# Performance work log

Measured on AMD Instinct MI355X. Metric: run time of the kernel, lower is better.

## Reference

```python
import jax, jax.numpy as jnp
import numpy as np

B, N, HID = 8, 1024, 768
HEADS, LORA, HDIM = 12, 256, 64


def setup_inputs() -> dict:
    key = jax.random.key(0)
    k1, k2, k3 = jax.random.split(key, 3)
    hidden_states = jax.random.normal(k1, (B, N, HID), dtype=jnp.float32)
    attention_mask = jnp.ones((B, N), dtype=jnp.int32)
    # torch Linear weights are [out_features, in_features]
    Wt = jax.random.normal(k2, (HEADS, LORA, HID), dtype=jnp.float32) * (HID ** -0.5)
    Wa = jax.random.normal(k3, (HEADS, HDIM, LORA), dtype=jnp.float32) * (LORA ** -0.5)
    return {"hidden_states": hidden_states, "attention_mask": attention_mask,
            "Wt": Wt, "Wa": Wa}


def reference(hidden_states, attention_mask, Wt, Wa):
    # Per-head LoRA projection, batched over heads instead of a Python loop.
    # t: [b, h, n, head_dim]; repeat(1,1,3) in the original makes q = k = v = t.
    scale = hidden_states.shape[-1] ** -0.5  # input_dim ** -0.5
    t = jnp.einsum('bnd,hld->bhnl', hidden_states, Wt)
    t = jnp.einsum('bhnl,hel->bhne', t, Wa)
    scores = jnp.einsum('bhid,bhjd->bhij', t, t) * scale
    scores = jnp.where(attention_mask[:, None, None, :] == 0, -jnp.inf, scores)
    attn = jax.nn.softmax(scores, axis=-1)
    out = jnp.einsum('bhij,bhjd->bhid', attn, t)  # [b, h, n, d]
    b, h, n, d = out.shape
    return out.transpose(0, 2, 1, 3).reshape(b, n, h * d)
```

## Files before the change

### kernel.cpp

```cpp
#include <hip/hip_runtime.h>
#include <math.h>

#define BATCH 8
#define SEQ   1024
#define HID_  768
#define HEADS 12
#define LORA  256
#define HDIM  64

#define SCALE      0.03608439182435161f
#define SCALE_LOG2 0.05205863235888918f

typedef _Float16 f16_t;
typedef _Float16 f16x2 __attribute__((ext_vector_type(2)));
typedef _Float16 f16x4 __attribute__((ext_vector_type(4)));
typedef _Float16 f16x8 __attribute__((ext_vector_type(8)));
typedef float    f32x4 __attribute__((ext_vector_type(4)));

#define GLD16(g, l) __builtin_amdgcn_global_load_lds( \
    (const __attribute__((address_space(1))) void*)(g), \
    (__attribute__((address_space(3))) void*)(l), 16, 0, 0)

#define SW(c, r) ((((c) ^ ((r) & 7)) << 3))

#define N4_HS (BATCH * SEQ * HID_ / 4)

__global__ __launch_bounds__(256) void prep_kernel(
    const float4* __restrict__ hs, const float* __restrict__ Wt,
    const float* __restrict__ Wa, f16x4* __restrict__ hs_f,
    f16_t* __restrict__ w_f)
{
    __shared__ float s_a[64][68];
    __shared__ float s_b[64][36];

    const int tid = threadIdx.x;

    if (blockIdx.x >= 288) {
        int i0 = (blockIdx.x - 288) * 256 + tid;
        int stride = (gridDim.x - 288) * 256;
        for (int i = i0; i < N4_HS; i += stride) {
            float4 v = hs[i];
            f16x4 o = {(f16_t)v.x, (f16_t)v.y, (f16_t)v.z, (f16_t)v.w};
            hs_f[i] = o;
        }
        return;
    }

    const int bid = blockIdx.x;
    const int h   = bid / 24;
    const int d0  = (bid % 24) * 32;
    const int ty  = tid >> 4;
    const int tx  = tid & 15;

    const float* wa_g = Wa + (size_t)h * HDIM * LORA;
    const float* wt_g = Wt + (size_t)h * LORA * HID_;

    float acc[4][2] = {{0.f, 0.f}, {0.f, 0.f}, {0.f, 0.f}, {0.f, 0.f}};

    for (int kc = 0; kc < 4; ++kc) {
        const int l0 = kc * 64;
        if (kc) __syncthreads();
        #pragma unroll
        for (int k = 0; k < 4; ++k) {
            int u = tid + k * 256;
            int r = u >> 4, c4 = (u & 15) * 4;
            *(float4*)&s_a[r][c4] = *(const float4*)&wa_g[(size_t)r * LORA + l0 + c4];
        }
        #pragma unroll
        for (int k = 0; k < 2; ++k) {
            int u = tid + k * 256;
            int r = u >> 3, c4 = (u & 7) * 4;
            *(float4*)&s_b[r][c4] = *(const float4*)&wt_g[(size_t)(l0 + r) * HID_ + d0 + c4];
        }
        __syncthreads();

        #pragma unroll 8
        for (int l = 0; l < 64; ++l) {
            float a0 = s_a[ty * 4 + 0][l];
            float a1 = s_a[ty * 4 + 1][l];
            float a2 = s_a[ty * 4 + 2][l];
            float a3 = s_a[ty * 4 + 3][l];
            float b0 = s_b[l][tx * 2 + 0];
            float b1 = s_b[l][tx * 2 + 1];
            acc[0][0] = fmaf(a0, b0, acc[0][0]); acc[0][1] = fmaf(a0, b1, acc[0][1]);
            acc[1][0] = fmaf(a1, b0, acc[1][0]); acc[1][1] = fmaf(a1, b1, acc[1][1]);
            acc[2][0] = fmaf(a2, b0, acc[2][0]); acc[2][1] = fmaf(a2, b1, acc[2][1]);
            acc[3][0] = fmaf(a3, b0, acc[3][0]); acc[3][1] = fmaf(a3, b1, acc[3][1]);
        }
    }

    f16_t* wg = w_f + (size_t)h * HDIM * HID_;
    #pragma unroll
    for (int i = 0; i < 4; ++i) {
        int e = ty * 4 + i;
        f16x2 o = {(f16_t)acc[i][0], (f16_t)acc[i][1]};
        *(f16x2*)&wg[(size_t)e * HID_ + d0 + tx * 2] = o;
    }
}

__global__ __launch_bounds__(256, 3) void gemm_t(
    const f16_t* __restrict__ hs_f, const f16_t* __restrict__ w_f,
    f16_t* __restrict__ t_f, f16_t* __restrict__ tT_f)
{
    __shared__ __attribute__((aligned(16))) char smem[49152];
    f16_t* s_hs = (f16_t*)smem;
    f16_t* s_wt = (f16_t*)(smem + 32768);
    f16_t* s_ob = (f16_t*)smem;

    const int bid   = blockIdx.x;
    const int ntile = bid & 7;
    const int h     = (bid >> 3) % HEADS;
    const int b     = bid / (8 * HEADS);
    const int n0    = ntile * 128;
    const int tid   = threadIdx.x;
    const int w     = tid >> 6;
    const int lane  = tid & 63;
    const int q     = lane >> 4;
    const int mr    = lane & 15;
    const int lrow  = lane >> 3;
    const int gswz  = (((lane & 7) ^ lrow) & 7) * 8;

    const f16_t* hs_g = hs_f + ((size_t)b * SEQ + n0) * HID_;
    const f16_t* w_g  = w_f + (size_t)h * HDIM * HID_;

    const f32x4 z4 = {0.f, 0.f, 0.f, 0.f};
    f32x4 acc[2][4];
    #pragma unroll
    for (int mt = 0; mt < 2; ++mt)
        #pragma unroll
        for (int et = 0; et < 4; ++et) acc[mt][et] = z4;

    auto STAGE = [&](int buf, int rd) {
        const int k0 = rd * 64;
        f16_t* sa = s_hs + buf * (128 * 64);
        f16_t* sb = s_wt + buf * (64 * 64);
        #pragma unroll
        for (int tt = 0; tt < 4; ++tt) {
            int r0 = w * 32 + tt * 8;
            GLD16(hs_g + (size_t)(r0 + lrow) * HID_ + k0 + gswz, sa + r0 * 64);
        }
        #pragma unroll
        for (int tt = 0; tt < 2; ++tt) {
            int r0 = w * 16 + tt * 8;
            GLD16(w_g + (size_t)(r0 + lrow) * HID_ + k0 + gswz, sb + r0 * 64);
        }
    };

    auto COMPUTE = [&](int buf) {
        const f16_t* sa = s_hs + buf * (128 * 64);
        const f16_t* sb = s_wt + buf * (64 * 64);
        #pragma unroll
        for (int ks = 0; ks < 2; ++ks) {
            f16x8 a_[2], b_[4];
            #pragma unroll
            for (int mt = 0; mt < 2; ++mt)
                a_[mt] = *(const f16x8*)(sa + (w * 32 + mt * 16 + mr) * 64 + SW(ks * 4 + q, mr));
            #pragma unroll
            for (int et = 0; et < 4; ++et)
                b_[et] = *(const f16x8*)(sb + (et * 16 + mr) * 64 + SW(ks * 4 + q, mr));
            #pragma unroll
            for (int mt = 0; mt < 2; ++mt)
                #pragma unroll
                for (int et = 0; et < 4; ++et)
                    acc[mt][et] = __builtin_amdgcn_mfma_f32_16x16x32_f16(a_[mt], b_[et], acc[mt][et], 0, 0, 0);
        }
    };

    STAGE(0, 0);
    __syncthreads();
    #pragma unroll 1
    for (int rr = 0; rr < 6; ++rr) {
        STAGE(1, 2 * rr + 1);
        COMPUTE(0);
        __syncthreads();
        if (rr < 5) STAGE(0, 2 * rr + 2);
        COMPUTE(1);
        __syncthreads();
    }

    #pragma unroll
    for (int mt = 0; mt < 2; ++mt) {
        #pragma unroll
        for (int et = 0; et < 4; ++et) {
            #pragma unroll
            for (int r = 0; r < 4; ++r) {
                int row = w * 32 + mt * 16 + q * 4 + r;
                int col = et * 16 + mr;
                s_ob[row * 72 + col] = (f16_t)acc[mt][et][r];
            }
        }
    }
    __syncthreads();

    f16_t* tg = t_f + (((size_t)b * HEADS + h) * SEQ + n0) * HDIM;
    #pragma unroll
    for (int k = 0; k < 4; ++k) {
        int u = tid + k * 256;
        int row = u >> 3, c8 = (u & 7) * 8;
        *(f16x8*)&tg[row * 64 + c8] = *(const f16x8*)&s_ob[row * 72 + c8];
    }
    f16_t* tTg = tT_f + ((size_t)b * HEADS + h) * SEQ * HDIM;
    #pragma unroll
    for (int k = 0; k < 4; ++k) {
        int u = tid + k * 256;
        int e = u & 63, n8 = (u >> 6) * 8;
        f16x8 v;
        #pragma unroll
        for (int j = 0; j < 8; ++j) v[j] = s_ob[(n8 + j) * 72 + e];
        *(f16x8*)&tTg[(size_t)e * SEQ + n0 + n8] = v;
    }
}

__global__ __launch_bounds__(256, 3) void attn_mfma(
    const f16_t* __restrict__ t_f, const f16_t* __restrict__ tT_f,
    const int* __restrict__ mask, float* __restrict__ out)
{
    __shared__ __attribute__((aligned(16))) char smem[34816];
    f16_t* s_k = (f16_t*)smem;
    f16_t* s_v = (f16_t*)(smem + 8192);
    f16_t* s_p = (f16_t*)(smem + 16384);
    float* s_m = (float*)smem;

    const int bid  = blockIdx.x;
    const int bh   = bid % (BATCH * HEADS);
    const int it   = bid / (BATCH * HEADS);
    const int h    = bh % HEADS;
    const int b    = bh / HEADS;
    const int i0   = it * 128;
    const int tid  = threadIdx.x;
    const int w    = tid >> 6;
    const int lane = tid & 63;
    const int q    = lane >> 4;
    const int mr   = lane & 15;
    const int lrow = lane >> 3;
    const int gswz = (((lane & 7) ^ lrow) & 7) * 8;
    const int ih   = w >> 1;
    const int jh   = w & 1;

    const size_t bh_off = ((size_t)b * HEADS + h) * SEQ * HDIM;
    const f16_t* th = t_f + bh_off;
    const f16_t* vh = tT_f + bh_off;
    const int* mk = mask + (size_t)b * SEQ;

    f16x8 qf[4][2];
    #pragma unroll
    for (int mt = 0; mt < 4; ++mt)
        #pragma unroll
        for (int ks = 0; ks < 2; ++ks) {
            f16x8 v = *(const f16x8*)(th + (size_t)(i0 + ih * 64 + mt * 16 + mr) * 64
                                      + ks * 32 + q * 8);
            #pragma unroll
            for (int j = 0; j < 8; ++j) v[j] = v[j] * (f16_t)SCALE_LOG2;
            qf[mt][ks] = v;
        }

    const f32x4 z4 = {0.f, 0.f, 0.f, 0.f};
    float l_[4] = {0.f, 0.f, 0.f, 0.f};
    f32x4 oT[4][4];
    #pragma unroll
    for (int mt = 0; mt < 4; ++mt)
        #pragma unroll
        for (int et = 0; et < 4; ++et) oT[mt][et] = z4;

    for (int jt6 = 0; jt6 < 16; ++jt6) {
        const int j0 = jt6 * 64;
        __syncthreads();
        #pragma unroll
        for (int t2 = 0; t2 < 2; ++t2) {
            int r0 = w * 16 + t2 * 8;
            GLD16(th + (size_t)(j0 + r0 + lrow) * 64 + gswz,  s_k + r0 * 64);
            GLD16(vh + (size_t)(r0 + lrow) * SEQ + j0 + gswz, s_v + r0 * 64);
        }
        __syncthreads();

        #pragma unroll
        for (int jt = 0; jt < 2; ++jt) {
            int4 mv = *(const int4*)(mk + j0 + jh * 32 + jt * 16 + q * 4);
            f32x4 bias = {(mv.x == 0) ? -60000.f : 0.f,
                          (mv.y == 0) ? -60000.f : 0.f,
                          (mv.z == 0) ? -60000.f : 0.f,
                          (mv.w == 0) ? -60000.f : 0.f};
            f32x4 st[4] = {bias, bias, bias, bias};
            __builtin_amdgcn_s_setprio(1);
            #pragma unroll
            for (int ks = 0; ks < 2; ++ks) {
                f16x8 kf = *(const f16x8*)(s_k + (jh * 32 + jt * 16 + mr) * 64 + SW(ks * 4 + q, mr));
                #pragma unroll
                for (int mt = 0; mt < 4; ++mt)
                    st[mt] = __builtin_amdgcn_mfma_f32_16x16x32_f16(kf, qf[mt][ks], st[mt], 0, 0, 0);
            }
            __builtin_amdgcn_s_setprio(0);
            #pragma unroll
            for (int mt = 0; mt < 4; ++mt) {
                float p0 = __builtin_amdgcn_exp2f(st[mt][0]);
                float p1 = __builtin_amdgcn_exp2f(st[mt][1]);
                float p2 = __builtin_amdgcn_exp2f(st[mt][2]);
                float p3 = __builtin_amdgcn_exp2f(st[mt][3]);
                l_[mt] += (p0 + p1) + (p2 + p3);
                f16x4 u4 = {(f16_t)p0, (f16_t)p1, (f16_t)p2, (f16_t)p3};
                *(f16x4*)&s_p[(ih * 64 + mt * 16 + mr) * 72 + jh * 32 + jt * 16 + q * 4] = u4;
            }
        }

        f16x8 pf[4];
        #pragma unroll
        for (int mt = 0; mt < 4; ++mt)
            pf[mt] = *(const f16x8*)(s_p + (ih * 64 + mt * 16 + mr) * 72 + jh * 32 + q * 8);
        __builtin_amdgcn_s_setprio(1);
        #pragma unroll
        for (int et = 0; et < 4; ++et) {
            f16x8 vv = *(const f16x8*)(s_v + (et * 16 + mr) * 64 + SW(jh * 4 + q, mr));
            #pragma unroll
            for (int mt = 0; mt < 4; ++mt)
                oT[mt][et] = __builtin_amdgcn_mfma_f32_16x16x32_f16(vv, pf[mt], oT[mt][et], 0, 0, 0);
        }
        __builtin_amdgcn_s_setprio(0);
    }

    #pragma unroll
    for (int mt = 0; mt < 4; ++mt) {
        l_[mt] += __shfl_xor(l_[mt], 16);
        l_[mt] += __shfl_xor(l_[mt], 32);
    }

    __syncthreads();
    if (jh == 1) {
        float* dst = s_m + ((size_t)ih * 64 + lane) * 68;
        #pragma unroll
        for (int mt = 0; mt < 4; ++mt) {
            #pragma unroll
            for (int et = 0; et < 4; ++et)
                *(f32x4*)&dst[(mt * 4 + et) * 4] = oT[mt][et];
            dst[64 + mt] = l_[mt];
        }
    }
    __syncthreads();
    if (jh == 0) {
        const float* src = s_m + ((size_t)ih * 64 + lane) * 68;
        #pragma unroll
        for (int mt = 0; mt < 4; ++mt) {
            float lt = l_[mt] + src[64 + mt];
            float inv = (lt > 0.f) ? 1.f / lt : 0.f;
            int n = i0 + ih * 64 + mt * 16 + mr;
            #pragma unroll
            for (int et = 0; et < 4; ++et) {
                f32x4 o2 = *(const f32x4*)&src[(mt * 4 + et) * 4];
                float4 v = {(oT[mt][et][0] + o2[0]) * inv, (oT[mt][et][1] + o2[1]) * inv,
                            (oT[mt][et][2] + o2[2]) * inv, (oT[mt][et][3] + o2[3]) * inv};
                *(float4*)&out[((size_t)b * SEQ + n) * (HEADS * HDIM) + h * HDIM + et * 16 + q * 4] = v;
            }
        }
    }
}

extern "C" void kernel_launch(void* const* d_in, const int* in_sizes, int n_in,
                              void* d_out, int out_size, void* d_ws, size_t ws_size,
                              hipStream_t stream) {
    const float* hs   = (const float*)d_in[0];
    const int*   mask = (const int*)d_in[1];
    const float* Wt   = (const float*)d_in[2];
    const float* Wa   = (const float*)d_in[3];
    float* out = (float*)d_out;

    char* ws = (char*)d_ws;
    f16_t* t_f  = (f16_t*)ws;
    f16_t* tT_f = (f16_t*)(ws + 12582912);
    f16_t* hs_f = (f16_t*)(ws + 25165824);
    f16_t* w_f  = (f16_t*)(ws + 37748736);

    prep_kernel<<<288 + 1024, 256, 0, stream>>>(
        (const float4*)hs, Wt, Wa, (f16x4*)hs_f, w_f);

    gemm_t<<<BATCH * HEADS * (SEQ / 128), 256, 0, stream>>>(hs_f, w_f, t_f, tT_f);

    attn_mfma<<<BATCH * HEADS * (SEQ / 128), 256, 0, stream>>>(
        t_f, tT_f, mask, out);
}
```

Measured before the change: 150.2 us.

## Fuse prep, projection GEMM and attention into one persistent kernel with grid barriers

Replaces three separate kernel launches with a single 768-block kernel whose phases are separated by software grid-wide barriers built on atomic counters, plus a memset that resets the counters. The aim is to remove launch gaps and inter-kernel drain between the stages. In exchange, every stage now runs on a fixed 768-block grid. The prep stage loses the extra 1024 conversion blocks, and shared memory is sized to the largest phase, which can limit occupancy. The barrier also relies on all blocks being co-resident, so it can deadlock or time out if they are not.

Result: slower. 506.0 us (+236.8%).

```diff
diff --git a/kernel.cpp b/kernel.cpp
--- a/kernel.cpp
+++ b/kernel.cpp
@@ -7,6 +7,7 @@
 #define HEADS 12
 #define LORA  256
 #define HDIM  64
+#define GRID_ 768
 
 #define SCALE      0.03608439182435161f
 #define SCALE_LOG2 0.05205863235888918f
@@ -25,329 +26,341 @@
 
 #define N4_HS (BATCH * SEQ * HID_ / 4)
 
-__global__ __launch_bounds__(256) void prep_kernel(
-    const float4* __restrict__ hs, const float* __restrict__ Wt,
-    const float* __restrict__ Wa, f16x4* __restrict__ hs_f,
-    f16_t* __restrict__ w_f)
+__device__ __forceinline__ void grid_bar(unsigned* ctr) {
+    __threadfence();
+    __syncthreads();
+    if (threadIdx.x == 0) {
+        atomicAdd(ctr, 1u);
+        unsigned v = 0;
+        long guard = 0;
+        do {
+            v = __hip_atomic_load(ctr, __ATOMIC_RELAXED, __HIP_MEMORY_SCOPE_AGENT);
+            if (v >= GRID_) break;
+            __builtin_amdgcn_s_sleep(8);
+        } while (++guard < 100000000L);
+    }
+    __syncthreads();
+    __threadfence();
+}
+
+__global__ __launch_bounds__(256, 3) void mega_kernel(
+    const float4* __restrict__ hs4, const float* __restrict__ Wt,
+    const float* __restrict__ Wa, const int* __restrict__ mask,
+    float* __restrict__ out, f16_t* __restrict__ t_f,
+    f16_t* __restrict__ tT_f, f16_t* __restrict__ hs_f,
+    f16_t* __restrict__ w_f, unsigned* __restrict__ bars)
 {
-    __shared__ float s_a[64][68];
-    __shared__ float s_b[64][36];
-
+    __shared__ __attribute__((aligned(16))) char smem[49152];
+
+    const int bid = blockIdx.x;
     const int tid = threadIdx.x;
 
-    if (blockIdx.x >= 288) {
-        int i0 = (blockIdx.x - 288) * 256 + tid;
-        int stride = (gridDim.x - 288) * 256;
-        for (int i = i0; i < N4_HS; i += stride) {
-            float4 v = hs[i];
-            f16x4 o = {(f16_t)v.x, (f16_t)v.y, (f16_t)v.z, (f16_t)v.w};
-            hs_f[i] = o;
-        }
-        return;
+    {
+        if (bid < 288) {
+            float* s_a = (float*)smem;
+            float* s_b = (float*)(smem + 17408);
+            const int h   = bid / 24;
+            const int d0  = (bid % 24) * 32;
+            const int ty  = tid >> 4;
+            const int tx  = tid & 15;
+
+            const float* wa_g = Wa + (size_t)h * HDIM * LORA;
+            const float* wt_g = Wt + (size_t)h * LORA * HID_;
+
+            float acc[4][2] = {{0.f, 0.f}, {0.f, 0.f}, {0.f, 0.f}, {0.f, 0.f}};
+
+            for (int kc = 0; kc < 4; ++kc) {
+                const int l0 = kc * 64;
+                if (kc) __syncthreads();
+                #pragma unroll
+                for (int k = 0; k < 4; ++k) {
+                    int u = tid + k * 256;
+                    int r = u >> 4, c4 = (u & 15) * 4;
+                    *(float4*)&s_a[r * 68 + c4] = *(const float4*)&wa_g[(size_t)r * LORA + l0 + c4];
+                }
+                #pragma unroll
+                for (int k = 0; k < 2; ++k) {
+                    int u = tid + k * 256;
+                    int r = u >> 3, c4 = (u & 7) * 4;
+                    *(float4*)&s_b[r * 36 + c4] = *(const float4*)&wt_g[(size_t)(l0 + r) * HID_ + d0 + c4];
+                }
+                __syncthreads();
+
+                #pragma unroll 8
+                for (int l = 0; l < 64; ++l) {
+                    float a0 = s_a[(ty * 4 + 0) * 68 + l];
+                    float a1 = s_a[(ty * 4 + 1) * 68 + l];
+                    float a2 = s_a[(ty * 4 + 2) * 68 + l];
+                    float a3 = s_a[(ty * 4 + 3) * 68 + l];
+                    float b0 = s_b[l * 36 + tx * 2 + 0];
+                    float b1 = s_b[l * 36 + tx * 2 + 1];
+                    acc[0][0] = fmaf(a0, b0, acc[0][0]); acc[0][1] = fmaf(a0, b1, acc[0][1]);
+                    acc[1][0] = fmaf(a1, b0, acc[1][0]); acc[1][1] = fmaf(a1, b1, acc[1][1]);
+                    acc[2][0] = fmaf(a2, b0, acc[2][0]); acc[2][1] = fmaf(a2, b1, acc[2][1]);
+                    acc[3][0] = fmaf(a3, b0, acc[3][0]); acc[3][1] = fmaf(a3, b1, acc[3][1]);
+                }
+            }
+
+            f16_t* wg = w_f + (size_t)h * HDIM * HID_;
+            #pragma unroll
+            for (int i = 0; i < 4; ++i) {
+                int e = ty * 4 + i;
+                f16x2 o = {(f16_t)acc[i][0], (f16_t)acc[i][1]};
+                *(f16x2*)&wg[(size_t)e * HID_ + d0 + tx * 2] = o;
+            }
+        } else {
+            f16x4* hsf4 = (f16x4*)hs_f;
+            int i0 = (bid - 288) * 256 + tid;
+            int stride = (GRID_ - 288) * 256;
+            for (int i = i0; i < N4_HS; i += stride) {
+                float4 v = hs4[i];
+                f16x4 o = {(f16_t)v.x, (f16_t)v.y, (f16_t)v.z, (f16_t)v.w};
+                hsf4[i] = o;
+            }
+        }
     }
-
-    const int bid = blockIdx.x;
-    const int h   = bid / 24;
-    const int d0  = (bid % 24) * 32;
-    const int ty  = tid >> 4;
-    const int tx  = tid & 15;
-
-    const float* wa_g = Wa + (size_t)h * HDIM * LORA;
-    const float* wt_g = Wt + (size_t)h * LORA * HID_;
-
-    float acc[4][2] = {{0.f, 0.f}, {0.f, 0.f}, {0.f, 0.f}, {0.f, 0.f}};
-
-    for (int kc = 0; kc < 4; ++kc) {
-        const int l0 = kc * 64;
-        if (kc) __syncthreads();
+    grid_bar(&bars[0]);
+
+    {
+        f16_t* s_hs = (f16_t*)smem;
+        f16_t* s_wt = (f16_t*)(smem + 32768);
+        f16_t* s_ob = (f16_t*)smem;
+
+        const int ntile = bid & 7;
+        const int h     = (bid >> 3) % HEADS;
+        const int b     = bid / (8 * HEADS);
+        const int n0    = ntile * 128;
+        const int w     = tid >> 6;
+        const int lane  = tid & 63;
+        const int q     = lane >> 4;
+        const int mr    = lane & 15;
+        const int lrow  = lane >> 3;
+        const int gswz  = (((lane & 7) ^ lrow) & 7) * 8;
+
+        const f16_t* hs_g = hs_f + ((size_t)b * SEQ + n0) * HID_;
+        const f16_t* w_g  = w_f + (size_t)h * HDIM * HID_;
+
+        const f32x4 z4 = {0.f, 0.f, 0.f, 0.f};
+        f32x4 acc[2][4];
+        #pragma unroll
+        for (int mt = 0; mt < 2; ++mt)
+            #pragma unroll
+            for (int et = 0; et < 4; ++et) acc[mt][et] = z4;
+
+        auto STAGE = [&](int buf, int rd) {
+            const int k0 = rd * 64;
+            f16_t* sa = s_hs + buf * (128 * 64);
+            f16_t* sb = s_wt + buf * (64 * 64);
+            #pragma unroll
+            for (int tt = 0; tt < 4; ++tt) {
+                int r0 = w * 32 + tt * 8;
+                GLD16(hs_g + (size_t)(r0 + lrow) * HID_ + k0 + gswz, sa + r0 * 64);
+            }
+            #pragma unroll
+            for (int tt = 0; tt < 2; ++tt) {
+                int r0 = w * 16 + tt * 8;
+                GLD16(w_g + (size_t)(r0 + lrow) * HID_ + k0 + gswz, sb + r0 * 64);
+            }
+        };
+
+        auto COMPUTE = [&](int buf) {
+            const f16_t* sa = s_hs + buf * (128 * 64);
+            const f16_t* sb = s_wt + buf * (64 * 64);
+            #pragma unroll
+            for (int ks = 0; ks < 2; ++ks) {
+                f16x8 a_[2], b_[4];
+                #pragma unroll
+                for (int mt = 0; mt < 2; ++mt)
+                    a_[mt] = *(const f16x8*)(sa + (w * 32 + mt * 16 + mr) * 64 + SW(ks * 4 + q, mr));
+                #pragma unroll
+                for (int et = 0; et < 4; ++et)
+                    b_[et] = *(const f16x8*)(sb + (et * 16 + mr) * 64 + SW(ks * 4 + q, mr));
+                #pragma unroll
+                for (int mt = 0; mt < 2; ++mt)
+                    #pragma unroll
+                    for (int et = 0; et < 4; ++et)
+                        acc[mt][et] = __builtin_amdgcn_mfma_f32_16x16x32_f16(a_[mt], b_[et], acc[mt][et], 0, 0, 0);
+            }
+        };
+
+        STAGE(0, 0);
+        __syncthreads();
+        #pragma unroll 1
+        for (int rr = 0; rr < 6; ++rr) {
+            STAGE(1, 2 * rr + 1);
+            COMPUTE(0);
+            __syncthreads();
+            if (rr < 5) STAGE(0, 2 * rr + 2);
+            COMPUTE(1);
+            __syncthreads();
+        }
+
+        #pragma unroll
+        for (int mt = 0; mt < 2; ++mt) {
+            #pragma unroll
+            for (int et = 0; et < 4; ++et) {
+                #pragma unroll
+                for (int r = 0; r < 4; ++r) {
+                    int row = w * 32 + mt * 16 + q * 4 + r;
+                    int col = et * 16 + mr;
+                    s_ob[row * 72 + col] = (f16_t)acc[mt][et][r];
+                }
+            }
+        }
+        __syncthreads();
+
+        f16_t* tg = t_f + (((size_t)b * HEADS + h) * SEQ + n0) * HDIM;
         #pragma unroll
         for (int k = 0; k < 4; ++k) {
             int u = tid + k * 256;
-            int r = u >> 4, c4 = (u & 15) * 4;
-            *(float4*)&s_a[r][c4] = *(const float4*)&wa_g[(size_t)r * LORA + l0 + c4];
-        }
-        #pragma unroll
-        for (int k = 0; k < 2; ++k) {
+            int row = u >> 3, c8 = (u & 7) * 8;
+            *(f16x8*)&tg[row * 64 + c8] = *(const f16x8*)&s_ob[row * 72 + c8];
+        }
+        f16_t* tTg = tT_f + ((size_t)b * HEADS + h) * SEQ * HDIM;
+        #pragma unroll
+        for (int k = 0; k < 4; ++k) {
             int u = tid + k * 256;
-            int r = u >> 3, c4 = (u & 7) * 4;
-            *(float4*)&s_b[r][c4] = *(const float4*)&wt_g[(size_t)(l0 + r) * HID_ + d0 + c4];
-        }
+            int e = u & 63, n8 = (u >> 6) * 8;
+            f16x8 v;
+            #pragma unroll
+            for (int j = 0; j < 8; ++j) v[j] = s_ob[(n8 + j) * 72 + e];
+            *(f16x8*)&tTg[(size_t)e * SEQ + n0 + n8] = v;
+        }
+    }
+    grid_bar(&bars[1]);
+
+    {
+        f16_t* s_k = (f16_t*)smem;
+        f16_t* s_v = (f16_t*)(smem + 8192);
+        f16_t* s_p = (f16_t*)(smem + 16384);
+        float* s_m = (float*)smem;
+
+        const int bh   = bid % (BATCH * HEADS);
+        const int it   = bid / (BATCH * HEADS);
+        const int h    = bh % HEADS;
+        const int b    = bh / HEADS;
+        const int i0   = it * 128;
+        const int w    = tid >> 6;
+        const int lane = tid & 63;
+        const int q    = lane >> 4;
+        const int mr   = lane & 15;
+        const int lrow = lane >> 3;
+        const int gswz = (((lane & 7) ^ lrow) & 7) * 8;
+        const int ih   = w >> 1;
+        const int jh   = w & 1;
+
+        const size_t bh_off = ((size_t)b * HEADS + h) * SEQ * HDIM;
+        const f16_t* th = t_f + bh_off;
+        const f16_t* vh = tT_f + bh_off;
+        const int* mk = mask + (size_t)b * SEQ;
+
+        f16x8 qf[4][2];
+        #pragma unroll
+        for (int mt = 0; mt < 4; ++mt)
+            #pragma unroll
+            for (int ks = 0; ks < 2; ++ks) {
+                f16x8 v = *(const f16x8*)(th + (size_t)(i0 + ih * 64 + mt * 16 + mr) * 64
+                                          + ks * 32 + q * 8);
+                #pragma unroll
+                for (int j = 0; j < 8; ++j) v[j] = v[j] * (f16_t)SCALE_LOG2;
+                qf[mt][ks] = v;
+            }
+
+        const f32x4 z4 = {0.f, 0.f, 0.f, 0.f};
+        float l_[4] = {0.f, 0.f, 0.f, 0.f};
+        f32x4 oT[4][4];
+        #pragma unroll
+        for (int mt = 0; mt < 4; ++mt)
+            #pragma unroll
+            for (int et = 0; et < 4; ++et) oT[mt][et] = z4;
+
+        for (int jt6 = 0; jt6 < 16; ++jt6) {
+            const int j0 = jt6 * 64;
+            __syncthreads();
+            #pragma unroll
+            for (int t2 = 0; t2 < 2; ++t2) {
+                int r0 = w * 16 + t2 * 8;
+                GLD16(th + (size_t)(j0 + r0 + lrow) * 64 + gswz,  s_k + r0 * 64);
+                GLD16(vh + (size_t)(r0 + lrow) * SEQ + j0 + gswz, s_v + r0 * 64);
+            }
+            __syncthreads();
+
+            #pragma unroll
+            for (int jt = 0; jt < 2; ++jt) {
+                int4 mv = *(const int4*)(mk + j0 + jh * 32 + jt * 16 + q * 4);
+                f32x4 bias = {(mv.x == 0) ? -60000.f : 0.f,
+                              (mv.y == 0) ? -60000.f : 0.f,
+                              (mv.z == 0) ? -60000.f : 0.f,
+                              (mv.w == 0) ? -60000.f : 0.f};
+                f32x4 st[4] = {bias, bias, bias, bias};
+                __builtin_amdgcn_s_setprio(1);
+                #pragma unroll
+                for (int ks = 0; ks < 2; ++ks) {
+                    f16x8 kf = *(const f16x8*)(s_k + (jh * 32 + jt * 16 + mr) * 64 + SW(ks * 4 + q, mr));
+                    #pragma unroll
+                    for (int mt = 0; mt < 4; ++mt)
+                        st[mt] = __builtin_amdgcn_mfma_f32_16x16x32_f16(kf, qf[mt][ks], st[mt], 0, 0, 0);
+                }
+                __builtin_amdgcn_s_setprio(0);
+                #pragma unroll
+                for (int mt = 0; mt < 4; ++mt) {
+                    float p0 = __builtin_amdgcn_exp2f(st[mt][0]);
+                    float p1 = __builtin_amdgcn_exp2f(st[mt][1]);
+                    float p2 = __builtin_amdgcn_exp2f(st[mt][2]);
+                    float p3 = __builtin_amdgcn_exp2f(st[mt][3]);
+                    l_[mt] += (p0 + p1) + (p2 + p3);
+                    f16x4 u4 = {(f16_t)p0, (f16_t)p1, (f16_t)p2, (f16_t)p3};
+                    *(f16x4*)&s_p[(ih * 64 + mt * 16 + mr) * 72 + jh * 32 + jt * 16 + q * 4] = u4;
+                }
+            }
+
+            f16x8 pf[4];
+            #pragma unroll
+            for (int mt = 0; mt < 4; ++mt)
+                pf[mt] = *(const f16x8*)(s_p + (ih * 64 + mt * 16 + mr) * 72 + jh * 32 + q * 8);
+            __builtin_amdgcn_s_setprio(1);
+            #pragma unroll
+            for (int et = 0; et < 4; ++et) {
+                f16x8 vv = *(const f16x8*)(s_v + (et * 16 + mr) * 64 + SW(jh * 4 + q, mr));
+                #pragma unroll
+                for (int mt = 0; mt < 4; ++mt)
+                    oT[mt][et] = __builtin_amdgcn_mfma_f32_16x16x32_f16(vv, pf[mt], oT[mt][et], 0, 0, 0);
+            }
+            __builtin_amdgcn_s_setprio(0);
+        }
+
+        #pragma unroll
+        for (int mt = 0; mt < 4; ++mt) {
+            l_[mt] += __shfl_xor(l_[mt], 16);
+            l_[mt] += __shfl_xor(l_[mt], 32);
+        }
+
         __syncthreads();
-
-        #pragma unroll 8
-        for (int l = 0; l < 64; ++l) {
-            float a0 = s_a[ty * 4 + 0][l];
-            float a1 = s_a[ty * 4 + 1][l];
-            float a2 = s_a[ty * 4 + 2][l];
-            float a3 = s_a[ty * 4 + 3][l];
-            float b0 = s_b[l][tx * 2 + 0];
-            float b1 = s_b[l][tx * 2 + 1];
-            acc[0][0] = fmaf(a0, b0, acc[0][0]); acc[0][1] = fmaf(a0, b1, acc[0][1]);
-            acc[1][0] = fmaf(a1, b0, acc[1][0]); acc[1][1] = fmaf(a1, b1, acc[1][1]);
-            acc[2][0] = fmaf(a2, b0, acc[2][0]); acc[2][1] = fmaf(a2, b1, acc[2][1]);
-            acc[3][0] = fmaf(a3, b0, acc[3][0]); acc[3][1] = fmaf(a3, b1, acc[3][1]);
-        }
-    }
-
-    f16_t* wg = w_f + (size_t)h * HDIM * HID_;
-    #pragma unroll
-    for (int i = 0; i < 4; ++i) {
-        int e = ty * 4 + i;
-        f16x2 o = {(f16_t)acc[i][0], (f16_t)acc[i][1]};
-        *(f16x2*)&wg[(size_t)e * HID_ + d0 + tx * 2] = o;
-    }
-}
-
-__global__ __launch_bounds__(256, 3) void gemm_t(
-    const f16_t* __restrict__ hs_f, const f16_t* __restrict__ w_f,
-    f16_t* __restrict__ t_f, f16_t* __restrict__ tT_f)
-{
-    __shared__ __attribute__((aligned(16))) char smem[49152];
-    f16_t* s_hs = (f16_t*)smem;
-    f16_t* s_wt = (f16_t*)(smem + 32768);
-    f16_t* s_ob = (f16_t*)smem;
-
-    const int bid   = blockIdx.x;
-    const int ntile = bid & 7;
-    const int h     = (bid >> 3) % HEADS;
-    const int b     = bid / (8 * HEADS);
-    const int n0    = ntile * 128;
-    const int tid   = threadIdx.x;
-    const int w     = tid >> 6;
-    const int lane  = tid & 63;
-    const int q     = lane >> 4;
-    const int mr    = lane & 15;
-    const int lrow  = lane >> 3;
-    const int gswz  = (((lane & 7) ^ lrow) & 7) * 8;
-
-    const f16_t* hs_g = hs_f + ((size_t)b * SEQ + n0) * HID_;
-    const f16_t* w_g  = w_f + (size_t)h * HDIM * HID_;
-
-    const f32x4 z4 = {0.f, 0.f, 0.f, 0.f};
-    f32x4 acc[2][4];
-    #pragma unroll
-    for (int mt = 0; mt < 2; ++mt)
-        #pragma unroll
-        for (int et = 0; et < 4; ++et) acc[mt][et] = z4;
-
-    auto STAGE = [&](int buf, int rd) {
-        const int k0 = rd * 64;
-        f16_t* sa = s_hs + buf * (128 * 64);
-        f16_t* sb = s_wt + buf * (64 * 64);
-        #pragma unroll
-        for (int tt = 0; tt < 4; ++tt) {
-            int r0 = w * 32 + tt * 8;
-            GLD16(hs_g + (size_t)(r0 + lrow) * HID_ + k0 + gswz, sa + r0 * 64);
-        }
-        #pragma unroll
-        for (int tt = 0; tt < 2; ++tt) {
-            int r0 = w * 16 + tt * 8;
-            GLD16(w_g + (size_t)(r0 + lrow) * HID_ + k0 + gswz, sb + r0 * 64);
-        }
-    };
-
-    auto COMPUTE = [&](int buf) {
-        const f16_t* sa = s_hs + buf * (128 * 64);
-        const f16_t* sb = s_wt + buf * (64 * 64);
-        #pragma unroll
-        for (int ks = 0; ks < 2; ++ks) {
-            f16x8 a_[2], b_[4];
-            #pragma unroll
-            for (int mt = 0; mt < 2; ++mt)
-                a_[mt] = *(const f16x8*)(sa + (w * 32 + mt * 16 + mr) * 64 + SW(ks * 4 + q, mr));
-            #pragma unroll
-            for (int et = 0; et < 4; ++et)
-                b_[et] = *(const f16x8*)(sb + (et * 16 + mr) * 64 + SW(ks * 4 + q, mr));
-            #pragma unroll
-            for (int mt = 0; mt < 2; ++mt)
+        if (jh == 1) {
+            float* dst = s_m + ((size_t)ih * 64 + lane) * 68;
+            #pragma unroll
+            for (int mt = 0; mt < 4; ++mt) {
                 #pragma unroll
                 for (int et = 0; et < 4; ++et)
-                    acc[mt][et] = __builtin_amdgcn_mfma_f32_16x16x32_f16(a_[mt], b_[et], acc[mt][et], 0, 0, 0);
-        }
-    };
-
-    STAGE(0, 0);
-    __syncthreads();
-    #pragma unroll 1
-    for (int rr = 0; rr < 6; ++rr) {
-        STAGE(1, 2 * rr + 1);
-        COMPUTE(0);
+                    *(f32x4*)&dst[(mt * 4 + et) * 4] = oT[mt][et];
+                dst[64 + mt] = l_[mt];
+            }
+        }
         __syncthreads();
-        if (rr < 5) STAGE(0, 2 * rr + 2);
-        COMPUTE(1);
-        __syncthreads();
-    }
-
-    #pragma unroll
-    for (int mt = 0; mt < 2; ++mt) {
-        #pragma unroll
-        for (int et = 0; et < 4; ++et) {
-            #pragma unroll
-            for (int r = 0; r < 4; ++r) {
-                int row = w * 32 + mt * 16 + q * 4 + r;
-                int col = et * 16 + mr;
-                s_ob[row * 72 + col] = (f16_t)acc[mt][et][r];
-            }
-        }
-    }
-    __syncthreads();
-
-    f16_t* tg = t_f + (((size_t)b * HEADS + h) * SEQ + n0) * HDIM;
-    #pragma unroll
-    for (int k = 0; k < 4; ++k) {
-        int u = tid + k * 256;
-        int row = u >> 3, c8 = (u & 7) * 8;
-        *(f16x8*)&tg[row * 64 + c8] = *(const f16x8*)&s_ob[row * 72 + c8];
-    }
-    f16_t* tTg = tT_f + ((size_t)b * HEADS + h) * SEQ * HDIM;
-    #pragma unroll
-    for (int k = 0; k < 4; ++k) {
-        int u = tid + k * 256;
-        int e = u & 63, n8 = (u >> 6) * 8;
-        f16x8 v;
-        #pragma unroll
-        for (int j = 0; j < 8; ++j) v[j] = s_ob[(n8 + j) * 72 + e];
-        *(f16x8*)&tTg[(size_t)e * SEQ + n0 + n8] = v;
-    }
-}
-
-__global__ __launch_bounds__(256, 3) void attn_mfma(
-    const f16_t* __restrict__ t_f, const f16_t* __restrict__ tT_f,
-    const int* __restrict__ mask, float* __restrict__ out)
-{
-    __shared__ __attribute__((aligned(16))) char smem[34816];
-    f16_t* s_k = (f16_t*)smem;
-    f16_t* s_v = (f16_t*)(smem + 8192);
-    f16_t* s_p = (f16_t*)(smem + 16384);
-    float* s_m = (float*)smem;
-
-    const int bid  = blockIdx.x;
-    const int bh   = bid % (BATCH * HEADS);
-    const int it   = bid / (BATCH * HEADS);
-    const int h    = bh % HEADS;
-    const int b    = bh / HEADS;
-    const int i0   = it * 128;
-    const int tid  = threadIdx.x;
-    const int w    = tid >> 6;
-    const int lane = tid & 63;
-    const int q    = lane >> 4;
-    const int mr   = lane & 15;
-    const int lrow = lane >> 3;
-    const int gswz = (((lane & 7) ^ lrow) & 7) * 8;
-    const int ih   = w >> 1;
-    const int jh   = w & 1;
-
-    const size_t bh_off = ((size_t)b * HEADS + h) * SEQ * HDIM;
-    const f16_t* th = t_f + bh_off;
-    const f16_t* vh = tT_f + bh_off;
-    const int* mk = mask + (size_t)b * SEQ;
-
-    f16x8 qf[4][2];
-    #pragma unroll
-    for (int mt = 0; mt < 4; ++mt)
-        #pragma unroll
-        for (int ks = 0; ks < 2; ++ks) {
-            f16x8 v = *(const f16x8*)(th + (size_t)(i0 + ih * 64 + mt * 16 + mr) * 64
-                                      + ks * 32 + q * 8);
-            #pragma unroll
-            for (int j = 0; j < 8; ++j) v[j] = v[j] * (f16_t)SCALE_LOG2;
-            qf[mt][ks] = v;
-        }
-
-    const f32x4 z4 = {0.f, 0.f, 0.f, 0.f};
-    float l_[4] = {0.f, 0.f, 0.f, 0.f};
-    f32x4 oT[4][4];
-    #pragma unroll
-    for (int mt = 0; mt < 4; ++mt)
-        #pragma unroll
-        for (int et = 0; et < 4; ++et) oT[mt][et] = z4;
-
-    for (int jt6 = 0; jt6 < 16; ++jt6) {
-        const int j0 = jt6 * 64;
-        __syncthreads();
-        #pragma unroll
-        for (int t2 = 0; t2 < 2; ++t2) {
-            int r0 = w * 16 + t2 * 8;
-            GLD16(th + (size_t)(j0 + r0 + lrow) * 64 + gswz,  s_k + r0 * 64);
-            GLD16(vh + (size_t)(r0 + lrow) * SEQ + j0 + gswz, s_v + r0 * 64);
-        }
-        __syncthreads();
-
-        #pragma unroll
-        for (int jt = 0; jt < 2; ++jt) {
-            int4 mv = *(const int4*)(mk + j0 + jh * 32 + jt * 16 + q * 4);
-            f32x4 bias = {(mv.x == 0) ? -60000.f : 0.f,
-                          (mv.y == 0) ? -60000.f : 0.f,
-                          (mv.z == 0) ? -60000.f : 0.f,
-                          (mv.w == 0) ? -60000.f : 0.f};
-            f32x4 st[4] = {bias, bias, bias, bias};
-            __builtin_amdgcn_s_setprio(1);
-            #pragma unroll
-            for (int ks = 0; ks < 2; ++ks) {
-                f16x8 kf = *(const f16x8*)(s_k + (jh * 32 + jt * 16 + mr) * 64 + SW(ks * 4 + q, mr));
-                #pragma unroll
-                for (int mt = 0; mt < 4; ++mt)
-                    st[mt] = __builtin_amdgcn_mfma_f32_16x16x32_f16(kf, qf[mt][ks], st[mt], 0, 0, 0);
-            }
-            __builtin_amdgcn_s_setprio(0);
+        if (jh == 0) {
+            const float* src = s_m + ((size_t)ih * 64 + lane) * 68;
             #pragma unroll
             for (int mt = 0; mt < 4; ++mt) {
-                float p0 = __builtin_amdgcn_exp2f(st[mt][0]);
-                float p1 = __builtin_amdgcn_exp2f(st[mt][1]);
-                float p2 = __builtin_amdgcn_exp2f(st[mt][2]);
-                float p3 = __builtin_amdgcn_exp2f(st[mt][3]);
-                l_[mt] += (p0 + p1) + (p2 + p3);
-                f16x4 u4 = {(f16_t)p0, (f16_t)p1, (f16_t)p2, (f16_t)p3};
-                *(f16x4*)&s_p[(ih * 64 + mt * 16 + mr) * 72 + jh * 32 + jt * 16 + q * 4] = u4;
-            }
-        }
-
-        f16x8 pf[4];
-        #pragma unroll
-        for (int mt = 0; mt < 4; ++mt)
-            pf[mt] = *(const f16x8*)(s_p + (ih * 64 + mt * 16 + mr) * 72 + jh * 32 + q * 8);
-        __builtin_amdgcn_s_setprio(1);
-        #pragma unroll
-        for (int et = 0; et < 4; ++et) {
-            f16x8 vv = *(const f16x8*)(s_v + (et * 16 + mr) * 64 + SW(jh * 4 + q, mr));
-            #pragma unroll
-            for (int mt = 0; mt < 4; ++mt)
-                oT[mt][et] = __builtin_amdgcn_mfma_f32_16x16x32_f16(vv, pf[mt], oT[mt][et], 0, 0, 0);
-        }
-        __builtin_amdgcn_s_setprio(0);
-    }
-
-    #pragma unroll
-    for (int mt = 0; mt < 4; ++mt) {
-        l_[mt] += __shfl_xor(l_[mt], 16);
-        l_[mt] += __shfl_xor(l_[mt], 32);
-    }
-
-    __syncthreads();
-    if (jh == 1) {
-        float* dst = s_m + ((size_t)ih * 64 + lane) * 68;
-        #pragma unroll
-        for (int mt = 0; mt < 4; ++mt) {
-            #pragma unroll
-            for (int et = 0; et < 4; ++et)
-                *(f32x4*)&dst[(mt * 4 + et) * 4] = oT[mt][et];
-            dst[64 + mt] = l_[mt];
-        }
-    }
-    __syncthreads();
-    if (jh == 0) {
-        const float* src = s_m + ((size_t)ih * 64 + lane) * 68;
-        #pragma unroll
-        for (int mt = 0; mt < 4; ++mt) {
-            float lt = l_[mt] + src[64 + mt];
-            float inv = (lt > 0.f) ? 1.f / lt : 0.f;
-            int n = i0 + ih * 64 + mt * 16 + mr;
-            #pragma unroll
-            for (int et = 0; et < 4; ++et) {
-                f32x4 o2 = *(const f32x4*)&src[(mt * 4 + et) * 4];
-                float4 v = {(oT[mt][et][0] + o2[0]) * inv, (oT[mt][et][1] + o2[1]) * inv,
-                            (oT[mt][et][2] + o2[2]) * inv, (oT[mt][et][3] + o2[3]) * inv};
-                *(float4*)&out[((size_t)b * SEQ + n) * (HEADS * HDIM) + h * HDIM + et * 16 + q * 4] = v;
+                float lt = l_[mt] + src[64 + mt];
+                float inv = (lt > 0.f) ? 1.f / lt : 0.f;
+                int n = i0 + ih * 64 + mt * 16 + mr;
+                #pragma unroll
+                for (int et = 0; et < 4; ++et) {
+                    f32x4 o2 = *(const f32x4*)&src[(mt * 4 + et) * 4];
+                    float4 v = {(oT[mt][et][0] + o2[0]) * inv, (oT[mt][et][1] + o2[1]) * inv,
+                                (oT[mt][et][2] + o2[2]) * inv, (oT[mt][et][3] + o2[3]) * inv};
+                    *(float4*)&out[((size_t)b * SEQ + n) * (HEADS * HDIM) + h * HDIM + et * 16 + q * 4] = v;
+                }
             }
         }
     }
@@ -367,12 +380,10 @@
     f16_t* tT_f = (f16_t*)(ws + 12582912);
     f16_t* hs_f = (f16_t*)(ws + 25165824);
     f16_t* w_f  = (f16_t*)(ws + 37748736);
-
-    prep_kernel<<<288 + 1024, 256, 0, stream>>>(
-        (const float4*)hs, Wt, Wa, (f16x4*)hs_f, w_f);
-
-    gemm_t<<<BATCH * HEADS * (SEQ / 128), 256, 0, stream>>>(hs_f, w_f, t_f, tT_f);
-
-    attn_mfma<<<BATCH * HEADS * (SEQ / 128), 256, 0, stream>>>(
-        t_f, tT_f, mask, out);
+    unsigned* bars = (unsigned*)(ws + 38928384);
+
+    hipMemsetAsync(bars, 0, 2 * sizeof(unsigned), stream);
+
+    mega_kernel<<<GRID_, 256, 0, stream>>>(
+        (const float4*)hs, Wt, Wa, mask, out, t_f, tT_f, hs_f, w_f, bars);
 }
```

## Fuse fp32-to-fp16 hidden-state conversion into projection GEMM staging

Applied to the files above, without the earlier changes.

Removes the separate pass that converted the hidden states to an fp16 workspace buffer. The projection GEMM now loads fp32 hidden states directly with register loads, converts them to fp16, and writes them swizzled into LDS, while the weights still use async global-to-LDS loads. This saves a 25MB read plus a 12MB write of the intermediate. The cost is that each hidden-state tile is now read in fp32 by all 12 head blocks, and the register-staged path may serialize with compute instead of overlapping asynchronously.

New measurement: 155.9 us. +3.8%, slower.

```diff
diff --git a/kernel.cpp b/kernel.cpp
--- a/kernel.cpp
+++ b/kernel.cpp
@@ -23,29 +23,14 @@
 
 #define SW(c, r) ((((c) ^ ((r) & 7)) << 3))
 
-#define N4_HS (BATCH * SEQ * HID_ / 4)
-
 __global__ __launch_bounds__(256) void prep_kernel(
-    const float4* __restrict__ hs, const float* __restrict__ Wt,
-    const float* __restrict__ Wa, f16x4* __restrict__ hs_f,
+    const float* __restrict__ Wt, const float* __restrict__ Wa,
     f16_t* __restrict__ w_f)
 {
     __shared__ float s_a[64][68];
     __shared__ float s_b[64][36];
 
     const int tid = threadIdx.x;
-
-    if (blockIdx.x >= 288) {
-        int i0 = (blockIdx.x - 288) * 256 + tid;
-        int stride = (gridDim.x - 288) * 256;
-        for (int i = i0; i < N4_HS; i += stride) {
-            float4 v = hs[i];
-            f16x4 o = {(f16_t)v.x, (f16_t)v.y, (f16_t)v.z, (f16_t)v.w};
-            hs_f[i] = o;
-        }
-        return;
-    }
-
     const int bid = blockIdx.x;
     const int h   = bid / 24;
     const int d0  = (bid % 24) * 32;
@@ -99,7 +84,7 @@
 }
 
 __global__ __launch_bounds__(256, 3) void gemm_t(
-    const f16_t* __restrict__ hs_f, const f16_t* __restrict__ w_f,
+    const float* __restrict__ hs32, const f16_t* __restrict__ w_f,
     f16_t* __restrict__ t_f, f16_t* __restrict__ tT_f)
 {
     __shared__ __attribute__((aligned(16))) char smem[49152];
@@ -118,9 +103,10 @@
     const int q     = lane >> 4;
     const int mr    = lane & 15;
     const int lrow  = lane >> 3;
-    const int gswz  = (((lane & 7) ^ lrow) & 7) * 8;
-
-    const f16_t* hs_g = hs_f + ((size_t)b * SEQ + n0) * HID_;
+    const int lc    = lane & 7;
+    const int gswz  = ((lc ^ lrow) & 7) * 8;
+
+    const float* hs_g = hs32 + ((size_t)b * SEQ + n0) * HID_;
     const f16_t* w_g  = w_f + (size_t)h * HDIM * HID_;
 
     const f32x4 z4 = {0.f, 0.f, 0.f, 0.f};
@@ -135,14 +121,27 @@
         f16_t* sa = s_hs + buf * (128 * 64);
         f16_t* sb = s_wt + buf * (64 * 64);
         #pragma unroll
-        for (int tt = 0; tt < 4; ++tt) {
-            int r0 = w * 32 + tt * 8;
-            GLD16(hs_g + (size_t)(r0 + lrow) * HID_ + k0 + gswz, sa + r0 * 64);
-        }
-        #pragma unroll
         for (int tt = 0; tt < 2; ++tt) {
             int r0 = w * 16 + tt * 8;
             GLD16(w_g + (size_t)(r0 + lrow) * HID_ + k0 + gswz, sb + r0 * 64);
+        }
+        float4 va[4][2];
+        #pragma unroll
+        for (int tt = 0; tt < 4; ++tt) {
+            int row = w * 32 + tt * 8 + lrow;
+            const float* src = hs_g + (size_t)row * HID_ + k0 + lc * 8;
+            va[tt][0] = *(const float4*)(src);
+            va[tt][1] = *(const float4*)(src + 4);
+        }
+        #pragma unroll
+        for (int tt = 0; tt < 4; ++tt) {
+            int row = w * 32 + tt * 8 + lrow;
+            f16x8 o;
+            o[0] = (f16_t)va[tt][0].x; o[1] = (f16_t)va[tt][0].y;
+            o[2] = (f16_t)va[tt][0].z; o[3] = (f16_t)va[tt][0].w;
+            o[4] = (f16_t)va[tt][1].x; o[5] = (f16_t)va[tt][1].y;
+            o[6] = (f16_t)va[tt][1].z; o[7] = (f16_t)va[tt][1].w;
+            *(f16x8*)(sa + row * 64 + ((lc ^ lrow) << 3)) = o;
         }
     };
 
@@ -365,13 +364,11 @@
     char* ws = (char*)d_ws;
     f16_t* t_f  = (f16_t*)ws;
     f16_t* tT_f = (f16_t*)(ws + 12582912);
-    f16_t* hs_f = (f16_t*)(ws + 25165824);
-    f16_t* w_f  = (f16_t*)(ws + 37748736);
-
-    prep_kernel<<<288 + 1024, 256, 0, stream>>>(
-        (const float4*)hs, Wt, Wa, (f16x4*)hs_f, w_f);
-
-    gemm_t<<<BATCH * HEADS * (SEQ / 128), 256, 0, stream>>>(hs_f, w_f, t_f, tT_f);
+    f16_t* w_f  = (f16_t*)(ws + 25165824);
+
+    prep_kernel<<<HEADS * (HID_ / 32), 256, 0, stream>>>(Wt, Wa, w_f);
+
+    gemm_t<<<BATCH * HEADS * (SEQ / 128), 256, 0, stream>>>(hs, w_f, t_f, tT_f);
 
     attn_mfma<<<BATCH * HEADS * (SEQ / 128), 256, 0, stream>>>(
         t_f, tT_f, mask, out);
```
